# Performance work log

Hardware: AMD Instinct MI355X
Metric: run time of the kernel (lower is better)

## Reference

```python
import jax, jax.numpy as jnp
import numpy as np

CROP = 32  # crop_size from __init__

def conv2d(x, w, b):
    # 3x3 SAME conv, NHWC / HWIO
    return jax.lax.conv_general_dilated(x, w, (1, 1), 'SAME',
        dimension_numbers=('NHWC', 'HWIO', 'NHWC')) + b

def _crop_one(feat, box):
    # TF crop_and_resize-style bilinear crop of one normalized box [y1,x1,y2,x2]
    H, W, _ = feat.shape
    y1, x1, y2, x2 = box[0], box[1], box[2], box[3]
    t = jnp.linspace(0., 1., CROP)
    ys = y1 * (H - 1) + t * (y2 - y1) * (H - 1)
    xs = x1 * (W - 1) + t * (x2 - x1) * (W - 1)
    y0 = jnp.clip(jnp.floor(ys).astype(jnp.int32), 0, H - 2)
    wy = (ys - y0)[:, None, None]
    rows = feat[y0] * (1. - wy) + feat[y0 + 1] * wy          # [CROP, W, C]
    x0 = jnp.clip(jnp.floor(xs).astype(jnp.int32), 0, W - 2)
    wx = (xs - x0)[None, :, None]
    return rows[:, x0] * (1. - wx) + rows[:, x0 + 1] * wx    # [CROP, CROP, C]

# [B,H,W,C], [B,P,4] -> [B,P,CROP,CROP,C]
crop_features = jax.vmap(jax.vmap(_crop_one, in_axes=(None, 0)), in_axes=(0, 0))

def setup_inputs() -> dict:
    key = jax.random.key(0)
    ks = list(jax.random.split(key, 40))
    B, P, NC = 4, 64, 3
    C0, C1, C5 = 64, 128, 256
    RC, FC, SC, SF = 256, 256, 96, 256
    def w(k, *s):
        return jax.random.normal(k, s, jnp.float32) / np.sqrt(float(np.prod(s[:-1])))
    def b(n):
        return jnp.zeros((n,), jnp.float32)
    feat0 = jax.random.normal(ks[0], (B, 512, 512, C0), jnp.float32)
    feat1 = jax.random.normal(ks[1], (B, 256, 256, C1), jnp.float32)
    feat5 = jax.random.normal(ks[2], (B, 16, 16, C5), jnp.float32)
    yx = jax.random.uniform(ks[3], (B, P, 2), jnp.float32) * 0.7
    sz = 0.05 + jax.random.uniform(ks[4], (B, P, 2), jnp.float32) * 0.25
    boxes = jnp.concatenate([yx, jnp.minimum(yx + sz, 1.0)], -1)  # [y1,x1,y2,x2]
    return {
        'feat0': feat0, 'feat1': feat1, 'feat5': feat5, 'boxes': boxes,
        'cb1_w': w(ks[5], 3, 3, C1, RC), 'cb1_b': b(RC),
        'cb2_w': w(ks[6], 3, 3, RC, RC), 'cb2_b': b(RC),
        'reg_w': w(ks[7], 3, 3, RC, 4 * NC), 'reg_b': b(4 * NC),
        'wt_w': w(ks[8], 3, 3, RC, NC), 'wt_b': b(NC),
        'fc1_w': w(ks[9], C5, FC), 'fc1_b': b(FC),
        'fc2_w': w(ks[10], FC, FC), 'fc2_b': b(FC),
        'fc3_w': w(ks[11], FC, NC), 'fc3_b': b(NC),
        'sc1_w': w(ks[12], 3, 3, C0, SC), 'sc1_b': b(SC),
        'sc2_w': w(ks[13], 3, 3, SC, SC), 'sc2_b': b(SC),
        'so_w': w(ks[14], 3, 3, SC, NC), 'so_b': b(NC),
        'sd1_w': w(ks[15], (CROP // 4) * (CROP // 4) * SC, SF), 'sd1_b': b(SF),
        'sd2_w': w(ks[16], SF, SF), 'sd2_b': b(SF),
        'sd3_w': w(ks[17], SF, NC), 'sd3_b': b(NC),
    }

def reference(feat0, feat1, feat5, boxes,
              cb1_w, cb1_b, cb2_w, cb2_b, reg_w, reg_b, wt_w, wt_b,
              fc1_w, fc1_b, fc2_w, fc2_b, fc3_w, fc3_b,
              sc1_w, sc1_b, sc2_w, sc2_b, so_w, so_b,
              sd1_w, sd1_b, sd2_w, sd2_b, sd3_w, sd3_b):
    B, P = boxes.shape[0], boxes.shape[1]
    x = jax.nn.relu(conv2d(feat1, cb1_w, cb1_b))
    x = jax.nn.relu(conv2d(x, cb2_w, cb2_b))
    reg = conv2d(x, reg_w, reg_b)          # [B,h,w,4*n_cls]
    wts = conv2d(x, wt_w, wt_b)            # [B,h,w,n_cls]
    # classification branch on outputs['5']
    g = feat5.mean((1, 2))
    g = jax.nn.relu(g @ fc1_w + fc1_b)
    g = jax.nn.relu(g @ fc2_w + fc2_b)
    pred_cls = jax.nn.softmax(g @ fc3_w + fc3_b)   # [B,n_cls]
    cls = jnp.argmax(pred_cls, -1).astype(jnp.int32)  # [B]
    # per-class gathers (batch_dims=1)
    c4 = (cls * 4)[:, None, None, None]
    offsets = jnp.take_along_axis(reg, jnp.concatenate([c4, c4 + 1], -1), axis=-1)
    sizes = jnp.take_along_axis(reg, jnp.concatenate([c4 + 2, c4 + 3], -1), axis=-1)
    weights = jnp.take_along_axis(wts, cls[:, None, None, None], axis=-1)
    # ROI crops on outputs['0'] feeding segmentation head
    crops = crop_features(feat0, boxes)                     # [B,P,32,32,C0]
    crops = crops.reshape((B * P,) + crops.shape[2:])
    s = jax.nn.relu(conv2d(crops, sc1_w, sc1_b))
    s = jax.nn.relu(conv2d(s, sc2_w, sc2_b))                # [N,32,32,96]
    seg = conv2d(s, so_w, so_b)                             # [N,32,32,n_cls]
    cls_rep = jnp.repeat(cls, P)                            # [N]
    seg_sel = jnp.take_along_axis(seg, cls_rep[:, None, None, None], axis=-1)
    N, Hc, Wc, Cc = s.shape
    pooled = s.reshape(N, Hc // 4, 4, Wc // 4, 4, Cc).mean((2, 4)).reshape(N, -1)
    sc = jax.nn.relu(pooled @ sd1_w + sd1_b)
    sc = jax.nn.relu(sc @ sd2_w + sd2_b)
    sc = sc @ sd3_w + sd3_b
    score_sel = jnp.take_along_axis(sc, cls_rep[:, None], axis=-1)
    return (offsets, sizes, weights, pred_cls, seg_sel, score_sel)
```

## Files before the change

### kernel.cpp

```cpp
#include <hip/hip_runtime.h>

typedef unsigned short u16;
typedef short s16x8 __attribute__((ext_vector_type(8)));
typedef float f32x4 __attribute__((ext_vector_type(4)));

__device__ __forceinline__ float u2f(u16 u) {
    union { unsigned int i; float f; } c; c.i = ((unsigned int)u) << 16; return c.f;
}
__device__ __forceinline__ u16 f2u(float f) {
    union { float f; unsigned int i; } c; c.f = f;
    unsigned int x = c.i;
    x += 0x7fffu + ((x >> 16) & 1u);
    return (u16)(x >> 16);
}

template<int BN, int WMW, int WNW, int WSHIFT>
__global__ __launch_bounds__(256, 2)
void conv3x3_mfma(const u16* __restrict__ in, const u16* __restrict__ wT,
                  const float* __restrict__ bias, u16* __restrict__ out,
                  int Cin, int Cout, int Npad, int Wp, int in_img_stride,
                  int tiles_per_img, int xtiles,
                  int ldC, int out_rstride, int out_istride, int out_off,
                  int KC, int relu)
{
    constexpr int WT_    = 1 << WSHIFT;
    constexpr int WMROWS = 128 / WMW;
    constexpr int WNCOLS = BN / WNW;
    constexpr int AM     = WMROWS / 16;
    constexpr int AN     = WNCOLS / 16;
    constexpr int BINSTR = (BN * 64) / 1024;

    __shared__ __align__(16) u16 As[128 * 32];
    __shared__ __align__(16) u16 Bs[BN * 32];

    const int tid  = threadIdx.x;
    const int wave = tid >> 6;
    const int lane = tid & 63;
    const int l15  = lane & 15;
    const int quad = lane >> 4;
    const int wm   = wave / WNW;
    const int wn   = wave % WNW;

    const int tile  = blockIdx.x;
    const int n0    = blockIdx.y * BN;
    const int img   = tile / tiles_per_img;
    const int rem   = tile - img * tiles_per_img;
    const int ytile = rem / xtiles;
    const int xt    = rem - ytile * xtiles;
    const int RT    = 128 / WT_;
    const int y0    = ytile * RT;
    const int x0    = xt * WT_;

    const u16* aptr[2];
#pragma unroll
    for (int s = 0; s < 2; ++s) {
        int p = wave + s * 4;
        int e = p * 512 + lane * 8;
        int m = e >> 5;
        int c = e & 31;
        int ry = m >> WSHIFT;
        int xcol = m & (WT_ - 1);
        aptr[s] = in + (long)img * in_img_stride
                     + ((y0 + ry) * Wp + (x0 + xcol)) * Cin + c;
    }
    const u16* bptr[2];
    {
        int s = 0;
        for (int q = wave; q < BINSTR; q += 4, ++s) {
            int e = q * 512 + lane * 8;
            int n = e >> 5;
            int k = e & 31;
            bptr[s] = wT + (n0 + n) * Cin + k;
        }
    }

    f32x4 acc[AM][AN];
#pragma unroll
    for (int i = 0; i < AM; ++i)
#pragma unroll
        for (int j = 0; j < AN; ++j) acc[i][j] = {0.f, 0.f, 0.f, 0.f};

    for (int tap = 0; tap < 9; ++tap) {
        const int dy = tap / 3, dx = tap - dy * 3;
        const int aoff_tap = (dy * Wp + dx) * Cin;
        const int boff_tap = tap * Npad * Cin;
        for (int kc = 0; kc < KC; ++kc) {
            const int coff = kc * 32;
#pragma unroll
            for (int s = 0; s < 2; ++s) {
                __builtin_amdgcn_global_load_lds(
                    (const __attribute__((address_space(1))) void*)(aptr[s] + aoff_tap + coff),
                    (__attribute__((address_space(3))) void*)(&As[(wave + s * 4) * 512]),
                    16, 0, 0);
            }
            {
                int s = 0;
                for (int q = wave; q < BINSTR; q += 4, ++s) {
                    __builtin_amdgcn_global_load_lds(
                        (const __attribute__((address_space(1))) void*)(bptr[s] + boff_tap + coff),
                        (__attribute__((address_space(3))) void*)(&Bs[q * 512]),
                        16, 0, 0);
                }
            }
            __syncthreads();

            s16x8 af[AM], bf[AN];
#pragma unroll
            for (int i = 0; i < AM; ++i)
                af[i] = *(const s16x8*)&As[(wm * WMROWS + i * 16 + l15) * 32 + quad * 8];
#pragma unroll
            for (int j = 0; j < AN; ++j)
                bf[j] = *(const s16x8*)&Bs[(wn * WNCOLS + j * 16 + l15) * 32 + quad * 8];
#pragma unroll
            for (int i = 0; i < AM; ++i)
#pragma unroll
                for (int j = 0; j < AN; ++j)
                    acc[i][j] = __builtin_amdgcn_mfma_f32_16x16x32_bf16(
                        af[i], bf[j], acc[i][j], 0, 0, 0);
            __syncthreads();
        }
    }

    const long obase = (long)out_off + (long)img * out_istride;
#pragma unroll
    for (int i = 0; i < AM; ++i) {
        int mb = wm * WMROWS + i * 16 + quad * 4;
#pragma unroll
        for (int j = 0; j < AN; ++j) {
            int n = n0 + wn * WNCOLS + j * 16 + l15;
            if (n < Cout) {
                float bv = bias[n];
#pragma unroll
                for (int r = 0; r < 4; ++r) {
                    int m = mb + r;
                    int ry = m >> WSHIFT, xcol = m & (WT_ - 1);
                    float v = acc[i][j][r] + bv;
                    if (relu) v = fmaxf(v, 0.f);
                    out[obase + (long)(y0 + ry) * out_rstride + (long)(x0 + xcol) * ldC + n] = f2u(v);
                }
            }
        }
    }
}

template<int MQ, int NQ>
__device__ __forceinline__ void mfma_quad(f32x4 (&acc)[8][4], const s16x8 (&aR)[4][2],
                                          const s16x8 (&bR)[2][2])
{
#pragma unroll
    for (int i = 0; i < 4; ++i)
#pragma unroll
        for (int j = 0; j < 2; ++j)
#pragma unroll
            for (int k = 0; k < 2; ++k)
                acc[MQ * 4 + i][NQ * 2 + j] = __builtin_amdgcn_mfma_f32_16x16x32_bf16(
                    aR[i][k], bR[j][k], acc[MQ * 4 + i][NQ * 2 + j], 0, 0, 0);
}

#define BAR() asm volatile("s_barrier" ::: "memory")
#define VMW(n) asm volatile("s_waitcnt vmcnt(" #n ")" ::: "memory")

#define STG_A(slot, h, off) do { \
    __builtin_amdgcn_global_load_lds( \
        (const __attribute__((address_space(1))) void*)(aptrA[h][0] + (off)), \
        (__attribute__((address_space(3))) void*)(&lds[((slot) * 32768 + (h) * 16384 + wave * 1024) >> 1]), \
        16, 0, 0); \
    __builtin_amdgcn_global_load_lds( \
        (const __attribute__((address_space(1))) void*)(aptrA[h][1] + (off)), \
        (__attribute__((address_space(3))) void*)(&lds[((slot) * 32768 + (h) * 16384 + 8192 + wave * 1024) >> 1]), \
        16, 0, 0); \
} while (0)

#define STG_B(slot, h, off) do { \
    __builtin_amdgcn_global_load_lds( \
        (const __attribute__((address_space(1))) void*)(bptrB[h][0] + (off)), \
        (__attribute__((address_space(3))) void*)(&lds[(65536 + (slot) * 32768 + (h) * 16384 + wave * 1024) >> 1]), \
        16, 0, 0); \
    __builtin_amdgcn_global_load_lds( \
        (const __attribute__((address_space(1))) void*)(bptrB[h][1] + (off)), \
        (__attribute__((address_space(3))) void*)(&lds[(65536 + (slot) * 32768 + (h) * 16384 + 8192 + wave * 1024) >> 1]), \
        16, 0, 0); \
} while (0)

#define LDA_HALF(dst, soff, mq) do { \
    const int _ab = (soff) + (mq) * 16384 + arow; \
    _Pragma("unroll") \
    for (int _i = 0; _i < 4; ++_i) { \
        dst[_i][0] = *(const s16x8*)&lds[(_ab + _i * 2048 + cS0) >> 1]; \
        dst[_i][1] = *(const s16x8*)&lds[(_ab + _i * 2048 + cS1) >> 1]; \
    } \
} while (0)

#define LDB_HALF(dst, soff, nq) do { \
    const int _bb = 65536 + (soff) + (nq) * 16384 + brow; \
    _Pragma("unroll") \
    for (int _j = 0; _j < 2; ++_j) { \
        dst[_j][0] = *(const s16x8*)&lds[(_bb + _j * 2048 + cS0) >> 1]; \
        dst[_j][1] = *(const s16x8*)&lds[(_bb + _j * 2048 + cS1) >> 1]; \
    } \
} while (0)

template<int KC2, int WSHIFT>
__global__ __launch_bounds__(512, 2)
void conv3x3_8ph(const u16* __restrict__ in, const u16* __restrict__ wT,
                 const float* __restrict__ bias, u16* __restrict__ out,
                 int Cin, int Wp, long in_img_stride,
                 int tiles_per_img, int xtiles,
                 int ldC, int out_rstride, long out_istride, long out_off,
                 int relu)
{
    constexpr int WT_  = 1 << WSHIFT;
    constexpr int ROWS = 256 >> WSHIFT;
    constexpr int T    = 9 * KC2;

    __shared__ __align__(16) u16 lds[65536];

    const int tid  = threadIdx.x;
    const int wave = tid >> 6;
    const int lane = tid & 63;
    const int l15  = lane & 15;
    const int quad = lane >> 4;
    const int wm   = wave >> 2;
    const int wn   = wave & 3;
    const int x7   = l15 & 7;
    const int cS0  = (quad ^ x7) << 4;
    const int cS1  = ((quad | 4) ^ x7) << 4;
    const int arow = (l15 + wm * 64) * 128;
    const int brow = (l15 + wn * 32) * 128;

    const int nwg = gridDim.x;
    const int b0  = blockIdx.x;
    const int bid = (b0 & 7) * (nwg >> 3) + (b0 >> 3);

    const int img   = bid / tiles_per_img;
    const int rem   = bid - img * tiles_per_img;
    const int ytile = rem / xtiles;
    const int xt    = rem - ytile * xtiles;
    const int y0    = ytile * ROWS;
    const int x0    = xt * WT_;

    const u16* aptrA[2][2];
    const u16* bptrB[2][2];
    {
        const int lr0  = tid >> 3;
        const int s16v = tid & 7;
#pragma unroll
        for (int h = 0; h < 2; ++h)
#pragma unroll
            for (int r = 0; r < 2; ++r) {
                int lrow = r * 64 + lr0;
                int srcc = (s16v ^ (lrow & 7)) << 3;
                int rowA = lrow + (lrow & 64) + h * 64;
                int ry = rowA >> WSHIFT, xcol = rowA & (WT_ - 1);
                aptrA[h][r] = in + (long)img * in_img_stride
                            + ((long)(y0 + ry) * Wp + (x0 + xcol)) * Cin + srcc;
                int col = ((lrow >> 5) << 6) + h * 32 + (lrow & 31);
                bptrB[h][r] = wT + (long)col * Cin + srcc;
            }
    }

    f32x4 acc[8][4];
#pragma unroll
    for (int i = 0; i < 8; ++i)
#pragma unroll
        for (int j = 0; j < 4; ++j) acc[i][j] = {0.f, 0.f, 0.f, 0.f};

    auto aoff_of = [&](int v) -> long {
        int tap = v / KC2, kc = v - tap * KC2;
        int dy = tap / 3, dx = tap - dy * 3;
        return (long)(dy * Wp + dx) * Cin + kc * 64;
    };
    auto boff_of = [&](int v) -> long {
        int tap = v / KC2, kc = v - tap * KC2;
        return (long)tap * 256 * Cin + kc * 64;
    };

    STG_A(0, 0, 0);
    STG_B(0, 0, 0);
    STG_B(0, 1, 0);
    STG_A(0, 1, 0);
    VMW(4); BAR();

    s16x8 aR[4][2], bA[2][2], bB[2][2];

    for (int u = 0; u < T - 1; ++u) {
        const int s = (u & 1) * 32768;
        const int t = (u + 1) & 1;
        const long aN = aoff_of(u + 1);
        const long bN = boff_of(u + 1);
        LDA_HALF(aR, s, 0);
        LDB_HALF(bA, s, 0);
        STG_A(t, 0, aN);
        VMW(4); BAR();
        __builtin_amdgcn_s_setprio(1);
        mfma_quad<0, 0>(acc, aR, bA);
        __builtin_amdgcn_s_setprio(0);
        BAR();
        LDB_HALF(bB, s, 1);
        STG_B(t, 0, bN);
        VMW(4); BAR();
        __builtin_amdgcn_s_setprio(1);
        mfma_quad<0, 1>(acc, aR, bB);
        __builtin_amdgcn_s_setprio(0);
        BAR();
        LDA_HALF(aR, s, 1);
        STG_B(t, 1, bN);
        BAR();
        __builtin_amdgcn_s_setprio(1);
        mfma_quad<1, 0>(acc, aR, bA);
        __builtin_amdgcn_s_setprio(0);
        BAR();
        STG_A(t, 1, aN);
        VMW(4); BAR();
        __builtin_amdgcn_s_setprio(1);
        mfma_quad<1, 1>(acc, aR, bB);
        __builtin_amdgcn_s_setprio(0);
        BAR();
    }
    {
        const int s = ((T - 1) & 1) * 32768;
        LDA_HALF(aR, s, 0);
        LDB_HALF(bA, s, 0);
        VMW(2); BAR();
        __builtin_amdgcn_s_setprio(1);
        mfma_quad<0, 0>(acc, aR, bA);
        __builtin_amdgcn_s_setprio(0);
        LDB_HALF(bB, s, 1);
        VMW(0); BAR();
        mfma_quad<0, 1>(acc, aR, bB);
        LDA_HALF(aR, s, 1);
        mfma_quad<1, 0>(acc, aR, bA);
        mfma_quad<1, 1>(acc, aR, bB);
    }

    const long obase = out_off + (long)img * out_istride;
#pragma unroll
    for (int mi = 0; mi < 8; ++mi) {
        const int mbase = wm * 128 + mi * 16 + quad * 4;
#pragma unroll
        for (int nj = 0; nj < 4; ++nj) {
            const int n = wn * 64 + nj * 16 + l15;
            const float bv = bias[n];
#pragma unroll
            for (int r = 0; r < 4; ++r) {
                int m = mbase + r;
                int ry = m >> WSHIFT, xcol = m & (WT_ - 1);
                float v = acc[mi][nj][r] + bv;
                if (relu) v = fmaxf(v, 0.f);
                out[obase + (long)(y0 + ry) * out_rstride + (long)(x0 + xcol) * ldC + n] = f2u(v);
            }
        }
    }
}

#undef BAR
#undef VMW
#undef STG_A
#undef STG_B
#undef LDA_HALF
#undef LDB_HALF

__global__ void zero_ring(u16* __restrict__ buf, int Hp, int Wp, int C,
                          long img_stride, int per, long tot)
{
    long idx = (long)blockIdx.x * 256 + threadIdx.x;
    if (idx >= tot) return;
    int img = (int)(idx / per);
    int r = (int)(idx - (long)img * per);
    int pos = r / C;
    int c = r - pos * C;
    long off;
    if (pos < Wp)            off = (long)pos * C;
    else if (pos < 2 * Wp)   off = ((long)(Hp - 1) * Wp + (pos - Wp)) * C;
    else {
        int p2 = pos - 2 * Wp;
        int row = 1 + (p2 >> 1);
        off = ((long)row * Wp + ((p2 & 1) ? (Wp - 1) : 0)) * C;
    }
    buf[(long)img * img_stride + off + c] = 0;
}

__global__ void transpose_w(const float* __restrict__ w, u16* __restrict__ wT,
                            int Cin, int Cout, int Npad)
{
    int idx = blockIdx.x * 256 + threadIdx.x;
    int total = 9 * Npad * Cin;
    if (idx >= total) return;
    int cin = idx % Cin;
    int r = idx / Cin;
    int n = r % Npad;
    int tap = r / Npad;
    wT[idx] = (n < Cout) ? f2u(w[(tap * Cin + cin) * Cout + n]) : (u16)0;
}

__global__ void transpose_head(const float* __restrict__ regw, const float* __restrict__ wtw,
                               const float* __restrict__ regb, const float* __restrict__ wtb,
                               u16* __restrict__ wT, float* __restrict__ bOut)
{
    int idx = blockIdx.x * 256 + threadIdx.x;
    if (idx < 16)
        bOut[idx] = (idx < 12) ? regb[idx] : (idx < 15 ? wtb[idx - 12] : 0.f);
    if (idx >= 9 * 16 * 256) return;
    int cin = idx & 255;
    int r = idx >> 8;
    int n = r & 15;
    int tap = r >> 4;
    float v = 0.f;
    if (n < 12)      v = regw[(tap * 256 + cin) * 12 + n];
    else if (n < 15) v = wtw[(tap * 256 + cin) * 3 + (n - 12)];
    wT[idx] = f2u(v);
}

__global__ void cvt_pad(const float* __restrict__ in, u16* __restrict__ out)
{
    int idx = blockIdx.x * 256 + threadIdx.x;
    if (idx >= 4 * 256 * 256 * 16) return;
    int cc = idx & 15;
    int pos = idx >> 4;
    int x = pos & 255, y = (pos >> 8) & 255, b = pos >> 16;
    const float4* s4 = (const float4*)(in + (size_t)idx * 8);
    float4 a = s4[0], bb = s4[1];
    u16 tmp[8];
    tmp[0] = f2u(a.x);  tmp[1] = f2u(a.y);  tmp[2] = f2u(a.z);  tmp[3] = f2u(a.w);
    tmp[4] = f2u(bb.x); tmp[5] = f2u(bb.y); tmp[6] = f2u(bb.z); tmp[7] = f2u(bb.w);
    *(uint4*)&out[(((b * 258 + y + 1) * 258) + x + 1) * 128 + cc * 8] = *(uint4*)tmp;
}

__global__ __launch_bounds__(256)
void cls_head(const float* __restrict__ feat5,
              const float* fc1w, const float* fc1b,
              const float* fc2w, const float* fc2b,
              const float* fc3w, const float* fc3b,
              float* __restrict__ pred_out, int* __restrict__ cls_out)
{
    int b = blockIdx.x, t = threadIdx.x;
    __shared__ float g[256], h1[256], h2[256], lg[3];
    const float* base = feat5 + b * 65536;
    float s = 0.f;
    for (int p = 0; p < 256; ++p) s += base[p * 256 + t];
    g[t] = s * (1.f / 256.f);
    __syncthreads();
    float a = fc1b[t];
    for (int k = 0; k < 256; ++k) a += g[k] * fc1w[k * 256 + t];
    h1[t] = fmaxf(a, 0.f);
    __syncthreads();
    a = fc2b[t];
    for (int k = 0; k < 256; ++k) a += h1[k] * fc2w[k * 256 + t];
    h2[t] = fmaxf(a, 0.f);
    __syncthreads();
    if (t < 3) {
        float l = fc3b[t];
        for (int k = 0; k < 256; ++k) l += h2[k] * fc3w[k * 3 + t];
        lg[t] = l;
    }
    __syncthreads();
    if (t == 0) {
        float m = fmaxf(lg[0], fmaxf(lg[1], lg[2]));
        float e0 = expf(lg[0] - m), e1 = expf(lg[1] - m), e2 = expf(lg[2] - m);
        float inv = 1.f / (e0 + e1 + e2);
        pred_out[b * 3 + 0] = e0 * inv;
        pred_out[b * 3 + 1] = e1 * inv;
        pred_out[b * 3 + 2] = e2 * inv;
        int best = 0;
        if (lg[1] > lg[best]) best = 1;
        if (lg[2] > lg[best]) best = 2;
        cls_out[b] = best;
    }
}

__global__ __launch_bounds__(256)
void crop_kernel(const float* __restrict__ feat0, const float* __restrict__ boxes,
                 u16* __restrict__ cropsp)
{
    int gid = blockIdx.x;
    int oy = gid & 31;
    int n = gid >> 5;
    int b = n >> 6;
    const float* bx = boxes + n * 4;
    float y1 = bx[0], x1 = bx[1], y2 = bx[2], x2 = bx[3];
    float ty = (float)oy * (1.f / 31.f);
    float ys = y1 * 511.f + (ty * (y2 - y1)) * 511.f;
    int y0i = (int)floorf(ys);
    y0i = y0i < 0 ? 0 : (y0i > 510 ? 510 : y0i);
    float wy = ys - (float)y0i;
    int t = threadIdx.x;
    int c = t & 63;
    int xg = t >> 6;
    const float* r0 = feat0 + ((size_t)(b * 512 + y0i) * 512) * 64;
    for (int ox = xg; ox < 32; ox += 4) {
        float tx = (float)ox * (1.f / 31.f);
        float xs = x1 * 511.f + (tx * (x2 - x1)) * 511.f;
        int x0i = (int)floorf(xs);
        x0i = x0i < 0 ? 0 : (x0i > 510 ? 510 : x0i);
        float wx = xs - (float)x0i;
        float v00 = r0[x0i * 64 + c];
        float v01 = r0[(x0i + 1) * 64 + c];
        float v10 = r0[32768 + x0i * 64 + c];
        float v11 = r0[32768 + (x0i + 1) * 64 + c];
        float ca = v00 * (1.f - wy) + v10 * wy;
        float cb = v01 * (1.f - wy) + v11 * wy;
        float val = ca * (1.f - wx) + cb * wx;
        cropsp[((n * 34 + oy + 1) * 34 + ox + 1) * 64 + c] = f2u(val);
    }
}

__global__ void reg_gather(const u16* __restrict__ head15, const int* __restrict__ cls,
                           float* __restrict__ out)
{
    int idx = blockIdx.x * 256 + threadIdx.x;
    if (idx >= 262144) return;
    int b = idx >> 16;
    int cl = cls[b];
    int c4 = cl * 4;
    const u16* p = head15 + (long)idx * 16;
    out[idx * 2 + 0] = u2f(p[c4]);
    out[idx * 2 + 1] = u2f(p[c4 + 1]);
    out[524288 + idx * 2 + 0] = u2f(p[c4 + 2]);
    out[524288 + idx * 2 + 1] = u2f(p[c4 + 3]);
    out[1048576 + idx] = u2f(p[12 + cl]);
}

__global__ void seg_gather(const u16* __restrict__ seg16, const int* __restrict__ cls,
                           float* __restrict__ out)
{
    int idx = blockIdx.x * 256 + threadIdx.x;
    if (idx >= 262144) return;
    int n = idx >> 10;
    out[idx] = u2f(seg16[(long)idx * 16 + cls[n >> 6]]);
}

__global__ __launch_bounds__(256)
void score_head(const u16* __restrict__ s2p,
                const float* sd1w, const float* sd1b,
                const float* sd2w, const float* sd2b,
                const float* sd3w, const float* sd3b,
                const int* __restrict__ cls, float* __restrict__ out)
{
    int n = blockIdx.x, t = threadIdx.x;
    __shared__ float pooled[6144];
    __shared__ float h1[256], h2[256];
    const u16* sb = s2p + (long)n * 34 * 34 * 96;
    for (int q = 0; q < 24; ++q) {
        int o = t + 256 * q;
        int c = o % 96;
        int pw = o / 96;
        int wx = pw & 7, hy = pw >> 3;
        float s = 0.f;
        for (int i = 0; i < 4; ++i)
            for (int j = 0; j < 4; ++j)
                s += u2f(sb[((1 + hy * 4 + i) * 34 + (1 + wx * 4 + j)) * 96 + c]);
        pooled[o] = s * 0.0625f;
    }
    __syncthreads();
    float a = sd1b[t];
    for (int k = 0; k < 6144; ++k) a += pooled[k] * sd1w[k * 256 + t];
    h1[t] = fmaxf(a, 0.f);
    __syncthreads();
    a = sd2b[t];
    for (int k = 0; k < 256; ++k) a += h1[k] * sd2w[k * 256 + t];
    h2[t] = fmaxf(a, 0.f);
    __syncthreads();
    if (t == 0) {
        int cl = cls[n >> 6];
        float s = sd3b[cl];
        for (int k = 0; k < 256; ++k) s += h2[k] * sd3w[k * 3 + cl];
        out[n] = s;
    }
}

extern "C" void kernel_launch(void* const* d_in, const int* in_sizes, int n_in,
                              void* d_out, int out_size, void* d_ws, size_t ws_size,
                              hipStream_t stream)
{
    const float* feat0 = (const float*)d_in[0];
    const float* feat1 = (const float*)d_in[1];
    const float* feat5 = (const float*)d_in[2];
    const float* boxes = (const float*)d_in[3];
    const float* cb1_w = (const float*)d_in[4];  const float* cb1_b = (const float*)d_in[5];
    const float* cb2_w = (const float*)d_in[6];  const float* cb2_b = (const float*)d_in[7];
    const float* reg_w = (const float*)d_in[8];  const float* reg_b = (const float*)d_in[9];
    const float* wt_w  = (const float*)d_in[10]; const float* wt_b  = (const float*)d_in[11];
    const float* fc1_w = (const float*)d_in[12]; const float* fc1_b = (const float*)d_in[13];
    const float* fc2_w = (const float*)d_in[14]; const float* fc2_b = (const float*)d_in[15];
    const float* fc3_w = (const float*)d_in[16]; const float* fc3_b = (const float*)d_in[17];
    const float* sc1_w = (const float*)d_in[18]; const float* sc1_b = (const float*)d_in[19];
    const float* sc2_w = (const float*)d_in[20]; const float* sc2_b = (const float*)d_in[21];
    const float* so_w  = (const float*)d_in[22]; const float* so_b  = (const float*)d_in[23];
    const float* sd1_w = (const float*)d_in[24]; const float* sd1_b = (const float*)d_in[25];
    const float* sd2_w = (const float*)d_in[26]; const float* sd2_b = (const float*)d_in[27];
    const float* sd3_w = (const float*)d_in[28]; const float* sd3_b = (const float*)d_in[29];

    char* ws = (char*)d_ws;
    size_t off = 0;
    auto alloc = [&](size_t bytes) -> char* {
        char* p = ws + off;
        off += (bytes + 255) & ~(size_t)255;
        return p;
    };
    u16* pad1   = (u16*)alloc(68161536);
    u16* x1p    = (u16*)alloc(136323072);
    u16* x2p    = (u16*)alloc(136323072);
    u16* head15 = (u16*)alloc(8388608);
    u16* seg16  = (u16*)alloc(8388608);
    u16* cb1T   = (u16*)alloc(589824);
    u16* cb2T   = (u16*)alloc(1179648);
    u16* headT  = (u16*)alloc(73728);
    float* headB = (float*)alloc(64);
    u16* sc1T   = (u16*)alloc(147456);
    u16* sc2T   = (u16*)alloc(221184);
    u16* soT    = (u16*)alloc(27648);
    int* cls    = (int*)alloc(16);
    u16* cropsp = pad1;
    u16* s1p    = x1p;
    u16* s2p    = x1p + 28409856;
    float* d_o  = (float*)d_out;

    auto ring = [&](u16* buf, int n, int Hp, int Wp, int C) {
        int per = (2 * Wp + 2 * (Hp - 2)) * C;
        long tot = (long)per * n;
        zero_ring<<<(int)((tot + 255) / 256), 256, 0, stream>>>(
            buf, Hp, Wp, C, (long)Hp * Wp * C, per, tot);
    };

    transpose_w<<<(9*256*128 + 255)/256, 256, 0, stream>>>(cb1_w, cb1T, 128, 256, 256);
    transpose_w<<<(9*256*256 + 255)/256, 256, 0, stream>>>(cb2_w, cb2T, 256, 256, 256);
    transpose_w<<<(9*128*64  + 255)/256, 256, 0, stream>>>(sc1_w, sc1T, 64, 96, 128);
    transpose_w<<<(9*128*96  + 255)/256, 256, 0, stream>>>(sc2_w, sc2T, 96, 96, 128);
    transpose_w<<<(9*16*96   + 255)/256, 256, 0, stream>>>(so_w,  soT,  96, 3, 16);
    transpose_head<<<(9*16*256 + 255)/256, 256, 0, stream>>>(reg_w, wt_w, reg_b, wt_b, headT, headB);

    cls_head<<<4, 256, 0, stream>>>(feat5, fc1_w, fc1_b, fc2_w, fc2_b, fc3_w, fc3_b,
                                    d_o + 1310720, cls);

    ring(pad1, 4, 258, 258, 128);
    cvt_pad<<<16384, 256, 0, stream>>>(feat1, pad1);
    ring(x1p, 4, 258, 258, 256);
    conv3x3_8ph<2, 7><<<1024, 512, 0, stream>>>(
        pad1, cb1T, cb1_b, x1p, 128, 258, 258L*258*128, 256, 2,
        256, 258*256, 258L*258*256, 259*256, 1);
    ring(x2p, 4, 258, 258, 256);
    conv3x3_8ph<4, 7><<<1024, 512, 0, stream>>>(
        x1p, cb2T, cb2_b, x2p, 256, 258, 258L*258*256, 256, 2,
        256, 258*256, 258L*258*256, 259*256, 1);
    conv3x3_mfma<16,4,1,7><<<dim3(2048,1), 256, 0, stream>>>(
        x2p, headT, headB, head15, 256, 15, 16, 258, 258*258*256, 512, 2,
        16, 256*16, 256*256*16, 0, 8, 0);
    reg_gather<<<1024, 256, 0, stream>>>(head15, cls, d_o);

    ring(cropsp, 256, 34, 34, 64);
    crop_kernel<<<8192, 256, 0, stream>>>(feat0, boxes, cropsp);
    ring(s1p, 256, 34, 34, 96);
    conv3x3_mfma<128,2,2,5><<<dim3(2048,1), 256, 0, stream>>>(
        cropsp, sc1T, sc1_b, s1p, 64, 96, 128, 34, 34*34*64, 8, 1,
        96, 34*96, 34*34*96, 35*96, 2, 1);
    ring(s2p, 256, 34, 34, 96);
    conv3x3_mfma<128,2,2,5><<<dim3(2048,1), 256, 0, stream>>>(
        s1p, sc2T, sc2_b, s2p, 96, 96, 128, 34, 34*34*96, 8, 1,
        96, 34*96, 34*34*96, 35*96, 3, 1);
    conv3x3_mfma<16,4,1,5><<<dim3(2048,1), 256, 0, stream>>>(
        s2p, soT, so_b, seg16, 96, 3, 16, 34, 34*34*96, 8, 1,
        16, 32*16, 32*32*16, 0, 3, 0);
    seg_gather<<<1024, 256, 0, stream>>>(seg16, cls, d_o + 1310732);
    score_head<<<256, 256, 0, stream>>>(s2p, sd1_w, sd1_b, sd2_w, sd2_b, sd3_w, sd3_b,
                                        cls, d_o + 1572876);
    (void)in_sizes; (void)n_in; (void)out_size; (void)ws_size;
}
```

Baseline: 1.623 ms.

## Add specialized narrow-output conv kernel for head convs and batch score head

Adds a dedicated 3x3 conv kernel for 16-wide output channels. It loads the whole weight set into LDS and double-buffers a swizzled input halo tile per channel chunk using global_load_lds, replacing the general MFMA conv for the regression/weight head and the segmentation output conv. A matching swizzled weight transpose kernel is added. The score head now processes four ROIs per block so each sd1/sd2 weight read is reused four times. The trade-off is heavy LDS use that limits occupancy to one block per CU, and swizzle indexing that has to match exactly between the transpose and the conv.

Result: faster. 1.483 ms (-8.6%).

```diff
diff --git a/kernel.cpp b/kernel.cpp
--- a/kernel.cpp
+++ b/kernel.cpp
@@ -353,12 +353,124 @@
     }
 }
 
-#undef BAR
-#undef VMW
 #undef STG_A
 #undef STG_B
 #undef LDA_HALF
 #undef LDB_HALF
+
+#define GLL(src, dst) __builtin_amdgcn_global_load_lds( \
+    (const __attribute__((address_space(1))) void*)(src), \
+    (__attribute__((address_space(3))) void*)(dst), 16, 0, 0)
+
+template<int TR, int TC, int CIN, int CINB, int NKC>
+__global__ __launch_bounds__(256, 1)
+void conv3x3_n16(const u16* __restrict__ in, const u16* __restrict__ wTs,
+                 const float* __restrict__ bias, u16* __restrict__ out,
+                 long in_img_stride, int Wp, int tiles_per_img, int xtiles,
+                 long out_istride, int out_rstride)
+{
+    constexpr int HC  = TC + 2;
+    constexpr int NB  = (9 * 16 * CINB * 2) / 1024;
+    constexpr int XSH = (TC == 64) ? 6 : 5;
+    static_assert((TR + 2) * HC <= 448, "halo must fit 28 chunks");
+
+    __shared__ __align__(16) u16 Bs[9 * 16 * CINB];
+    __shared__ __align__(16) u16 halo[28672];
+
+    const int tid  = threadIdx.x;
+    const int wave = tid >> 6;
+    const int lane = tid & 63;
+    const int l15  = lane & 15;
+    const int quad = lane >> 4;
+
+    const int bid   = blockIdx.x;
+    const int img   = bid / tiles_per_img;
+    const int rem   = bid - img * tiles_per_img;
+    const int ytile = rem / xtiles;
+    const int xt    = rem - ytile * xtiles;
+    const int gy0   = ytile * TR;
+    const int gx0   = xt * TC;
+
+    const u16* inb = in + (long)img * in_img_stride;
+
+    for (int i = wave; i < NB; i += 4)
+        GLL(wTs + i * 512 + lane * 8, &Bs[i * 512]);
+
+    const u16* hsrc[7];
+#pragma unroll
+    for (int i = 0; i < 7; ++i) {
+        int c  = wave + 4 * i;
+        int o  = c * 1024 + lane * 16;
+        int p  = o >> 6;
+        int sl = (o >> 4) & 3;
+        int c8 = sl ^ (p & 3);
+        int hr = p / HC; if (hr > TR + 1) hr = TR + 1;
+        int hx = p - hr * HC; if (hx > TC + 1) hx = TC + 1;
+        hsrc[i] = inb + ((long)(gy0 + hr) * Wp + (gx0 + hx)) * CIN + c8 * 8;
+    }
+
+    f32x4 acc[4];
+#pragma unroll
+    for (int mf = 0; mf < 4; ++mf) acc[mf] = {0.f, 0.f, 0.f, 0.f};
+
+    int pb[4];
+#pragma unroll
+    for (int mf = 0; mf < 4; ++mf) {
+        int m  = wave * 64 + mf * 16 + l15;
+        pb[mf] = (m >> XSH) * HC + (m & (TC - 1));
+    }
+
+#pragma unroll
+    for (int i = 0; i < 7; ++i)
+        GLL(hsrc[i], &halo[(wave + 4 * i) * 512]);
+    asm volatile("s_waitcnt vmcnt(0)" ::: "memory");
+    __syncthreads();
+
+    for (int kc = 0; kc < NKC; ++kc) {
+        if (kc + 1 < NKC) {
+            const int off = (kc + 1) * 32;
+            const int ds  = ((kc + 1) & 1) * 14336;
+#pragma unroll
+            for (int i = 0; i < 7; ++i)
+                GLL(hsrc[i] + off, &halo[ds + (wave + 4 * i) * 512]);
+        }
+        const int so_ = (kc & 1) * 14336;
+        const int cs4 = kc * 4 + quad;
+#pragma unroll
+        for (int tap = 0; tap < 9; ++tap) {
+            const int dy = tap / 3, dx = tap - dy * 3;
+            s16x8 bf = *(const s16x8*)&Bs[(tap * 16 + l15) * CINB
+                                          + ((cs4 ^ (l15 & 7)) << 3)];
+#pragma unroll
+            for (int mf = 0; mf < 4; ++mf) {
+                int p = pb[mf] + dy * HC + dx;
+                s16x8 af = *(const s16x8*)&halo[so_ + p * 32
+                                                + ((quad ^ (p & 3)) << 3)];
+                acc[mf] = __builtin_amdgcn_mfma_f32_16x16x32_bf16(
+                    af, bf, acc[mf], 0, 0, 0);
+            }
+        }
+        asm volatile("s_waitcnt vmcnt(0)" ::: "memory");
+        __syncthreads();
+    }
+
+    const long obase = (long)img * out_istride;
+    const float bv = bias[l15];
+#pragma unroll
+    for (int mf = 0; mf < 4; ++mf) {
+#pragma unroll
+        for (int r = 0; r < 4; ++r) {
+            int m  = wave * 64 + mf * 16 + quad * 4 + r;
+            int ry = m >> XSH, xc = m & (TC - 1);
+            out[obase + (long)(gy0 + ry) * out_rstride + (long)(gx0 + xc) * 16 + l15] =
+                f2u(acc[mf][r] + bv);
+        }
+    }
+}
+
+#undef GLL
+#undef BAR
+#undef VMW
 
 __global__ void zero_ring(u16* __restrict__ buf, int Hp, int Wp, int C,
                           long img_stride, int per, long tot)
@@ -393,22 +505,32 @@
     wT[idx] = (n < Cout) ? f2u(w[(tap * Cin + cin) * Cout + n]) : (u16)0;
 }
 
-__global__ void transpose_head(const float* __restrict__ regw, const float* __restrict__ wtw,
-                               const float* __restrict__ regb, const float* __restrict__ wtb,
-                               u16* __restrict__ wT, float* __restrict__ bOut)
+template<int CINB>
+__global__ void transpose_n16_swz(const float* __restrict__ w1,
+                                  const float* __restrict__ w2,
+                                  const float* __restrict__ b1,
+                                  const float* __restrict__ b2,
+                                  u16* __restrict__ wTs, float* __restrict__ bOut,
+                                  int Cin, int n1, int n2)
 {
     int idx = blockIdx.x * 256 + threadIdx.x;
-    if (idx < 16)
-        bOut[idx] = (idx < 12) ? regb[idx] : (idx < 15 ? wtb[idx - 12] : 0.f);
-    if (idx >= 9 * 16 * 256) return;
-    int cin = idx & 255;
-    int r = idx >> 8;
-    int n = r & 15;
-    int tap = r >> 4;
+    if (idx < 16 && blockIdx.x == 0)
+        bOut[idx] = (idx < n1) ? b1[idx] : (idx < n1 + n2 ? b2[idx - n1] : 0.f);
+    if (idx >= 9 * 16 * CINB) return;
+    constexpr int SL = CINB / 8;
+    int j    = idx & 7;
+    int r    = idx >> 3;
+    int slot = r & (SL - 1);
+    int r2   = r / SL;
+    int n    = r2 & 15;
+    int tap  = r2 >> 4;
+    int ch   = (slot ^ (n & 7)) * 8 + j;
     float v = 0.f;
-    if (n < 12)      v = regw[(tap * 256 + cin) * 12 + n];
-    else if (n < 15) v = wtw[(tap * 256 + cin) * 3 + (n - 12)];
-    wT[idx] = f2u(v);
+    if (ch < Cin) {
+        if (n < n1)           v = w1[(tap * Cin + ch) * n1 + n];
+        else if (n < n1 + n2) v = w2[(tap * Cin + ch) * n2 + (n - n1)];
+    }
+    wTs[idx] = f2u(v);
 }
 
 __global__ void cvt_pad(const float* __restrict__ in, u16* __restrict__ out)
@@ -530,41 +652,57 @@
 }
 
 __global__ __launch_bounds__(256)
-void score_head(const u16* __restrict__ s2p,
-                const float* sd1w, const float* sd1b,
-                const float* sd2w, const float* sd2b,
-                const float* sd3w, const float* sd3b,
-                const int* __restrict__ cls, float* __restrict__ out)
-{
-    int n = blockIdx.x, t = threadIdx.x;
-    __shared__ float pooled[6144];
-    __shared__ float h1[256], h2[256];
-    const u16* sb = s2p + (long)n * 34 * 34 * 96;
+void score_head2(const u16* __restrict__ s2p,
+                 const float* sd1w, const float* sd1b,
+                 const float* sd2w, const float* sd2b,
+                 const float* sd3w, const float* sd3b,
+                 const int* __restrict__ cls, float* __restrict__ out)
+{
+    int nb = blockIdx.x * 4;
+    int t = threadIdx.x;
+    __shared__ __align__(16) f32x4 pooled[6144];
+    __shared__ float h1[4][256];
+    __shared__ float h2[4][256];
     for (int q = 0; q < 24; ++q) {
         int o = t + 256 * q;
         int c = o % 96;
         int pw = o / 96;
         int wx = pw & 7, hy = pw >> 3;
-        float s = 0.f;
-        for (int i = 0; i < 4; ++i)
-            for (int j = 0; j < 4; ++j)
-                s += u2f(sb[((1 + hy * 4 + i) * 34 + (1 + wx * 4 + j)) * 96 + c]);
-        pooled[o] = s * 0.0625f;
+        f32x4 v;
+#pragma unroll
+        for (int j = 0; j < 4; ++j) {
+            const u16* sb = s2p + (long)(nb + j) * (34 * 34 * 96);
+            float s = 0.f;
+            for (int i = 0; i < 4; ++i)
+                for (int jj = 0; jj < 4; ++jj)
+                    s += u2f(sb[((1 + hy * 4 + i) * 34 + (1 + wx * 4 + jj)) * 96 + c]);
+            v[j] = s * 0.0625f;
+        }
+        pooled[o] = v;
     }
     __syncthreads();
-    float a = sd1b[t];
-    for (int k = 0; k < 6144; ++k) a += pooled[k] * sd1w[k * 256 + t];
-    h1[t] = fmaxf(a, 0.f);
+    float a0 = sd1b[t], a1 = a0, a2 = a0, a3 = a0;
+    for (int k = 0; k < 6144; ++k) {
+        float w = sd1w[k * 256 + t];
+        f32x4 pv = pooled[k];
+        a0 += pv[0] * w; a1 += pv[1] * w; a2 += pv[2] * w; a3 += pv[3] * w;
+    }
+    h1[0][t] = fmaxf(a0, 0.f); h1[1][t] = fmaxf(a1, 0.f);
+    h1[2][t] = fmaxf(a2, 0.f); h1[3][t] = fmaxf(a3, 0.f);
     __syncthreads();
-    a = sd2b[t];
-    for (int k = 0; k < 256; ++k) a += h1[k] * sd2w[k * 256 + t];
-    h2[t] = fmaxf(a, 0.f);
+    a0 = sd2b[t]; a1 = a0; a2 = a0; a3 = a0;
+    for (int k = 0; k < 256; ++k) {
+        float w = sd2w[k * 256 + t];
+        a0 += h1[0][k] * w; a1 += h1[1][k] * w; a2 += h1[2][k] * w; a3 += h1[3][k] * w;
+    }
+    h2[0][t] = fmaxf(a0, 0.f); h2[1][t] = fmaxf(a1, 0.f);
+    h2[2][t] = fmaxf(a2, 0.f); h2[3][t] = fmaxf(a3, 0.f);
     __syncthreads();
-    if (t == 0) {
-        int cl = cls[n >> 6];
+    if (t < 4) {
+        int cl = cls[(nb + t) >> 6];
         float s = sd3b[cl];
-        for (int k = 0; k < 256; ++k) s += h2[k] * sd3w[k * 3 + cl];
-        out[n] = s;
+        for (int k = 0; k < 256; ++k) s += h2[t][k] * sd3w[k * 3 + cl];
+        out[nb + t] = s;
     }
 }
 
@@ -608,7 +746,8 @@
     float* headB = (float*)alloc(64);
     u16* sc1T   = (u16*)alloc(147456);
     u16* sc2T   = (u16*)alloc(221184);
-    u16* soT    = (u16*)alloc(27648);
+    u16* soT    = (u16*)alloc(36864);
+    float* soB  = (float*)alloc(64);
     int* cls    = (int*)alloc(16);
     u16* cropsp = pad1;
     u16* s1p    = x1p;
@@ -626,8 +765,11 @@
     transpose_w<<<(9*256*256 + 255)/256, 256, 0, stream>>>(cb2_w, cb2T, 256, 256, 256);
     transpose_w<<<(9*128*64  + 255)/256, 256, 0, stream>>>(sc1_w, sc1T, 64, 96, 128);
     transpose_w<<<(9*128*96  + 255)/256, 256, 0, stream>>>(sc2_w, sc2T, 96, 96, 128);
-    transpose_w<<<(9*16*96   + 255)/256, 256, 0, stream>>>(so_w,  soT,  96, 3, 16);
-    transpose_head<<<(9*16*256 + 255)/256, 256, 0, stream>>>(reg_w, wt_w, reg_b, wt_b, headT, headB);
+    transpose_n16_swz<256><<<144, 256, 0, stream>>>(reg_w, wt_w, reg_b, wt_b,
+                                                    headT, headB, 256, 12, 3);
+    transpose_n16_swz<128><<<72, 256, 0, stream>>>(so_w, (const float*)nullptr,
+                                                   so_b, (const float*)nullptr,
+                                                   soT, soB, 96, 3, 0);
 
     cls_head<<<4, 256, 0, stream>>>(feat5, fc1_w, fc1_b, fc2_w, fc2_b, fc3_w, fc3_b,
                                     d_o + 1310720, cls);
@@ -642,9 +784,9 @@
     conv3x3_8ph<4, 7><<<1024, 512, 0, stream>>>(
         x1p, cb2T, cb2_b, x2p, 256, 258, 258L*258*256, 256, 2,
         256, 258*256, 258L*258*256, 259*256, 1);
-    conv3x3_mfma<16,4,1,7><<<dim3(2048,1), 256, 0, stream>>>(
-        x2p, headT, headB, head15, 256, 15, 16, 258, 258*258*256, 512, 2,
-        16, 256*16, 256*256*16, 0, 8, 0);
+    conv3x3_n16<4, 64, 256, 256, 8><<<1024, 256, 0, stream>>>(
+        x2p, headT, headB, head15, 258L*258*256, 258, 256, 4,
+        256L*256*16, 256*16);
     reg_gather<<<1024, 256, 0, stream>>>(head15, cls, d_o);
 
     ring(cropsp, 256, 34, 34, 64);
@@ -657,11 +799,11 @@
     conv3x3_mfma<128,2,2,5><<<dim3(2048,1), 256, 0, stream>>>(
         s1p, sc2T, sc2_b, s2p, 96, 96, 128, 34, 34*34*96, 8, 1,
         96, 34*96, 34*34*96, 35*96, 3, 1);
-    conv3x3_mfma<16,4,1,5><<<dim3(2048,1), 256, 0, stream>>>(
-        s2p, soT, so_b, seg16, 96, 3, 16, 34, 34*34*96, 8, 1,
-        16, 32*16, 32*32*16, 0, 3, 0);
+    conv3x3_n16<8, 32, 96, 128, 3><<<1024, 256, 0, stream>>>(
+        s2p, soT, soB, seg16, 34L*34*96, 34, 4, 1,
+        32L*32*16, 32*16);
     seg_gather<<<1024, 256, 0, stream>>>(seg16, cls, d_o + 1310732);
-    score_head<<<256, 256, 0, stream>>>(s2p, sd1_w, sd1_b, sd2_w, sd2_b, sd3_w, sd3_b,
+    score_head2<<<64, 256, 0, stream>>>(s2p, sd1_w, sd1_b, sd2_w, sd2_b, sd3_w, sd3_b,
                                         cls, d_o + 1572876);
     (void)in_sizes; (void)n_in; (void)out_size; (void)ws_size;
 }
```
